# Kernel tuning notes

Hardware: AMD Instinct MI355X
Metric: run time of the kernel (lower is better)

## Reference

```python
import jax, jax.numpy as jnp
import numpy as np

# --- config (Qwen3-Next linear attention defaults) ---
B, S, H = 1, 256, 2048
NK, NV, DK, DV, K = 4, 32, 128, 128, 4
KEY_DIM = NK * DK          # 512
VAL_DIM = NV * DV          # 4096
CONV_DIM = 2 * KEY_DIM + VAL_DIM  # 5120
EPS = 1e-6


def setup_inputs() -> dict:
    key = jax.random.key(0)
    ks = jax.random.split(key, 8)
    rn = lambda k, shape, sc: jax.random.normal(k, shape, jnp.float32) * sc
    return {
        "hidden_states": jax.random.normal(ks[0], (B, S, H), jnp.float32),
        "w_qkvz": rn(ks[1], (2 * KEY_DIM + 2 * VAL_DIM, H), 0.02),  # in_proj_qkvz weight
        "w_ba": rn(ks[2], (2 * NV, H), 0.02),                        # in_proj_ba weight
        "w_out": rn(ks[3], (H, VAL_DIM), 0.02),                      # out_proj weight
        "conv_w": rn(ks[4], (CONV_DIM, 1, K), 0.1),                  # depthwise conv weight [C,1,K]
        "dt_bias": jnp.ones((NV,), jnp.float32),
        "A_log": jnp.zeros((NV,), jnp.float32),
        "norm_w": jnp.ones((DV,), jnp.float32),
    }


def reference(hidden_states, w_qkvz, w_ba, w_out, conv_w, dt_bias, A_log, norm_w):
    b, s, _ = hidden_states.shape
    # input projections (Linear without bias: x @ W.T)
    qkvz = hidden_states @ w_qkvz.T                      # [B,S,9216]
    ba = hidden_states @ w_ba.T                          # [B,S,64]
    q, k, v, z = jnp.split(qkvz, [KEY_DIM, 2 * KEY_DIM, 2 * KEY_DIM + VAL_DIM], axis=-1)
    beta, alpha = jnp.split(ba, 2, axis=-1)              # each [B,S,NV]

    # causal depthwise conv over concat(q,k,v), then silu
    qkv = jnp.concatenate([q, k, v], axis=-1).transpose(0, 2, 1)   # [B,C,S]
    qkv = jax.lax.conv_general_dilated(
        qkv, conv_w, window_strides=(1,), padding=[(K - 1, 0)],
        dimension_numbers=("NCH", "OIH", "NCH"), feature_group_count=CONV_DIM)
    qkv = jax.nn.silu(qkv).transpose(0, 2, 1)            # [B,S,C]
    q, k, v = jnp.split(qkv, [KEY_DIM, 2 * KEY_DIM], axis=-1)

    q = q.reshape(b, s, NK, DK)
    k = k.reshape(b, s, NK, DK)
    v = v.reshape(b, s, NV, DV)
    z = z.reshape(b, s, NV, DV)

    # GQA-style head expansion (repeat_interleave)
    ratio = NV // NK
    q = jnp.repeat(q, ratio, axis=2)                     # [B,S,NV,DK]
    k = jnp.repeat(k, ratio, axis=2)

    # NOTE: original computes g = -softplus(-A_log - alpha) but never uses it (dead code).
    beta_g = jax.nn.sigmoid(beta + dt_bias)[..., None]   # [B,S,NV,1]
    q = q * (DK ** -0.5)

    # naive delta-rule: full outer-product tensor + cumsum (memory-bound)
    kv = jnp.einsum("bsnk,bsnv->bsnkv", k, v * beta_g)   # [B,S,NV,DK,DV]
    out = jnp.einsum("bsnk,bsnkv->bsnv", q, jnp.cumsum(kv, axis=1))  # [B,S,NV,DV]

    # gated RMSNorm over head_v_dim in fp32
    of = out.astype(jnp.float32)
    var = jnp.mean(of * of, axis=-1, keepdims=True)
    of = of * jax.lax.rsqrt(var + EPS) * norm_w
    of = of * jax.nn.silu(z.astype(jnp.float32))

    return of.reshape(b, s, VAL_DIM) @ w_out.T           # [B,S,H]
```

## Files before the change

kernel.cpp:

```cpp
#include <hip/hip_runtime.h>
#include <hip/hip_bf16.h>

#define S_LEN   256
#define HID     2048
#define NVH     32
#define DKD     128
#define DVD     128
#define KEYDIM  512
#define VALDIM  4096
#define CONVDIM 5120
#define QKVZ_N  9216
#define EPS_F   1e-6f

typedef __attribute__((ext_vector_type(8))) short bf16x8;
typedef __attribute__((ext_vector_type(4))) float f32x4;

__device__ __forceinline__ unsigned short f2bf(float f) {
    union { float f; unsigned int i; } v; v.f = f;
    unsigned int x = v.i;
    return (unsigned short)((x + 0x7FFFu + ((x >> 16) & 1u)) >> 16);
}
__device__ __forceinline__ unsigned int pk2(float x, float y) {
    union { __hip_bfloat162 h; unsigned int u; } c;
    c.h = __float22bfloat162_rn(float2{x, y});
    return c.u;
}
__device__ __forceinline__ bf16x8 pack_bf8(float4 lo, float4 hi) {
    union { uint4 u; bf16x8 h; } c;
    c.u.x = pk2(lo.x, lo.y); c.u.y = pk2(lo.z, lo.w);
    c.u.z = pk2(hi.x, hi.y); c.u.w = pk2(hi.z, hi.w);
    return c.h;
}
__device__ __forceinline__ void gl_lds16(const void* g, void* l) {
    __builtin_amdgcn_global_load_lds(
        (const __attribute__((address_space(1))) unsigned int*)g,
        (__attribute__((address_space(3))) unsigned int*)l,
        16, 0, 0);
}

template<int NT>
__global__ __launch_bounds__(256, 2)
void gemm_db(const unsigned short* __restrict__ A, const float* __restrict__ B,
             float* __restrict__ Cpart, int N, int K, int kc) {
    __shared__ __align__(16) unsigned short As[2][128][64];
    __shared__ __align__(16) float Bs[2][NT][64];

    const int tid  = threadIdx.x;
    const int lane = tid & 63, wave = tid >> 6;
    const int wm = wave >> 1, wn = wave & 1;
    const int quad = lane >> 4, l16 = lane & 15;
    const int m0 = blockIdx.y * 128, n0 = blockIdx.x * NT;
    const int kbeg = blockIdx.z * kc;
    const int niter = kc >> 6;

    const int a_ro = lane >> 3;
    const int a_gc = (lane & 7) ^ a_ro;
    const int b_ro = lane >> 4;
    const int b_cs = lane & 15;

    f32x4 acc[4][2];
#pragma unroll
    for (int i = 0; i < 4; i++)
#pragma unroll
        for (int j = 0; j < 2; j++) acc[i][j] = (f32x4){0.f, 0.f, 0.f, 0.f};

    auto stage = [&](int buf, int kk) {
#pragma unroll
        for (int t = 0; t < 4; ++t) {
            int rbase = wave * 32 + t * 8;
            gl_lds16(A + (size_t)(m0 + rbase + a_ro) * K + kk + a_gc * 8,
                     &As[buf][rbase][0]);
        }
#pragma unroll
        for (int t = 0; t < NT / 16; ++t) {
            int rbase = wave * (NT / 4) + t * 4;
            int r = rbase + b_ro;
            int gc = b_cs ^ (r & 7);
            gl_lds16(B + (size_t)(n0 + r) * K + kk + gc * 4,
                     &Bs[buf][rbase][0]);
        }
    };

    auto compute = [&](int buf) {
#pragma unroll
        for (int ks = 0; ks < 2; ++ks) {
            bf16x8 af[4];
#pragma unroll
            for (int i = 0; i < 4; ++i) {
                int r = wm * 64 + i * 16 + l16;
                int c = (ks * 4 + quad) ^ (l16 & 7);
                af[i] = *(const bf16x8*)(&As[buf][r][c * 8]);
            }
#pragma unroll
            for (int j = 0; j < 2; ++j) {
                int r = wn * 32 + j * 16 + l16;
                int x = l16 & 7;
                int c0 = (ks * 8 + quad * 2) ^ x;
                int c1 = (ks * 8 + quad * 2 + 1) ^ x;
                float4 lo = *(const float4*)(&Bs[buf][r][c0 * 4]);
                float4 hi = *(const float4*)(&Bs[buf][r][c1 * 4]);
                bf16x8 bfr = pack_bf8(lo, hi);
#pragma unroll
                for (int i = 0; i < 4; ++i)
                    acc[i][j] = __builtin_amdgcn_mfma_f32_16x16x32_bf16(af[i], bfr, acc[i][j], 0, 0, 0);
            }
        }
    };

    stage(0, kbeg);
    __syncthreads();
    for (int it = 0; it < niter; ++it) {
        if (it + 1 < niter) stage((it + 1) & 1, kbeg + (it + 1) * 64);
        compute(it & 1);
        __syncthreads();
    }

    float* C = Cpart + (size_t)blockIdx.z * 256 * N;
#pragma unroll
    for (int i = 0; i < 4; i++)
#pragma unroll
        for (int j = 0; j < 2; j++)
#pragma unroll
            for (int r = 0; r < 4; r++) {
                int row = m0 + wm * 64 + i * 16 + quad * 4 + r;
                int col = n0 + wn * 32 + j * 16 + l16;
                C[(size_t)row * N + col] = acc[i][j][r];
            }
}

template<int P>
__global__ void reduce_sum(const float* __restrict__ part, float* __restrict__ out, int n) {
    int i = (blockIdx.x * 256 + threadIdx.x) * 4;
    if (i >= n) return;
    float4 s = *(const float4*)(part + i);
#pragma unroll
    for (int p = 1; p < P; p++) {
        float4 v = *(const float4*)(part + (size_t)p * n + i);
        s.x += v.x; s.y += v.y; s.z += v.z; s.w += v.w;
    }
    *(float4*)(out + i) = s;
}

__global__ __launch_bounds__(256)
void ba_proj_cvt(const float* __restrict__ hs, const float* __restrict__ w_ba,
                 float* __restrict__ ba, unsigned short* __restrict__ abf) {
    int s = blockIdx.x;
    int n = threadIdx.x & 63, seg = threadIdx.x >> 6;
    const float* x = hs + (size_t)s * HID + seg * 512;
    const float* w = w_ba + (size_t)n * HID + seg * 512;
    float acc = 0.f;
#pragma unroll 4
    for (int k = 0; k < 512; k += 4) {
        float4 xv = *(const float4*)(x + k);
        float4 wv = *(const float4*)(w + k);
        acc += xv.x * wv.x + xv.y * wv.y + xv.z * wv.z + xv.w * wv.w;
    }
    __shared__ float parts[4][64];
    parts[seg][n] = acc;
    {
        int d = threadIdx.x * 8;
        const float4* p = (const float4*)(hs + (size_t)s * HID + d);
        float4 a = p[0], b = p[1];
        uint4 r;
        r.x = pk2(a.x, a.y); r.y = pk2(a.z, a.w);
        r.z = pk2(b.x, b.y); r.w = pk2(b.z, b.w);
        *(uint4*)(abf + (size_t)s * HID + d) = r;
    }
    __syncthreads();
    if (threadIdx.x < 64)
        ba[s * 64 + threadIdx.x] = parts[0][threadIdx.x] + parts[1][threadIdx.x]
                                 + parts[2][threadIdx.x] + parts[3][threadIdx.x];
}

template<int P>
__global__ __launch_bounds__(256)
void sum_conv(const float* __restrict__ part, const float* __restrict__ conv_w,
              float* __restrict__ conv, float* __restrict__ zs) {
    const int s0 = blockIdx.y * 16;
    const int c  = blockIdx.x * 1024 + threadIdx.x * 4;
    auto sum4 = [&](int s) {
        const float* p = part + (size_t)s * QKVZ_N + c;
        float4 v = *(const float4*)p;
#pragma unroll
        for (int q = 1; q < P; q++) {
            float4 w = *(const float4*)(p + (size_t)q * S_LEN * QKVZ_N);
            v.x += w.x; v.y += w.y; v.z += w.z; v.w += w.w;
        }
        return v;
    };
    if (c < CONVDIM) {
        float4 cw[4];
#pragma unroll
        for (int i = 0; i < 4; ++i) cw[i] = *(const float4*)(conv_w + (size_t)(c + i) * 4);
        float4 w0{0,0,0,0}, w1{0,0,0,0}, w2{0,0,0,0};
        for (int s = (s0 >= 3 ? s0 - 3 : 0); s < s0; ++s) { w0 = w1; w1 = w2; w2 = sum4(s); }
        for (int s = s0; s < s0 + 16; ++s) {
            float4 w3 = sum4(s);
            float4 o;
            o.x = w0.x * cw[0].x + w1.x * cw[0].y + w2.x * cw[0].z + w3.x * cw[0].w;
            o.y = w0.y * cw[1].x + w1.y * cw[1].y + w2.y * cw[1].z + w3.y * cw[1].w;
            o.z = w0.z * cw[2].x + w1.z * cw[2].y + w2.z * cw[2].z + w3.z * cw[2].w;
            o.w = w0.w * cw[3].x + w1.w * cw[3].y + w2.w * cw[3].z + w3.w * cw[3].w;
            o.x = o.x / (1.f + __expf(-o.x));
            o.y = o.y / (1.f + __expf(-o.y));
            o.z = o.z / (1.f + __expf(-o.z));
            o.w = o.w / (1.f + __expf(-o.w));
            *(float4*)(conv + (size_t)s * CONVDIM + c) = o;
            w0 = w1; w1 = w2; w2 = w3;
        }
    } else {
        for (int s = s0; s < s0 + 16; ++s) {
            float4 v = sum4(s);
            *(float4*)(zs + (size_t)s * VALDIM + (c - CONVDIM)) = v;
        }
    }
}

__global__ __launch_bounds__(256)
void scores_k(const float* __restrict__ conv, const float* __restrict__ ba,
              const float* __restrict__ dt_bias, float* __restrict__ scores) {
    if (blockIdx.x > blockIdx.y) return;
    int hk = blockIdx.z;
    int s0 = blockIdx.y * 16, t0 = blockIdx.x * 16;
    __shared__ float Qs[16][132], Ks[16][132];
    int tid = threadIdx.x;
    int qoff = hk * DKD;
    int koff = KEYDIM + hk * DKD;
    for (int idx = tid; idx < 16 * 128; idx += 256) {
        int i = idx >> 7, d = idx & 127;
        Qs[i][d] = conv[(size_t)(s0 + i) * CONVDIM + qoff + d];
        Ks[i][d] = conv[(size_t)(t0 + i) * CONVDIM + koff + d];
    }
    __syncthreads();
    int tx = tid & 15, ty = tid >> 4;
    int s = s0 + ty, t = t0 + tx;
    float dot = 0.f;
    for (int d = 0; d < 128; d++) dot += Qs[ty][d] * Ks[tx][d];
    float base = (t <= s) ? dot * 0.08838834764831845f : 0.f;
#pragma unroll
    for (int v = 0; v < 8; v++) {
        int n = hk * 8 + v;
        float b = ba[t * 64 + n] + dt_bias[n];
        float bg = 1.f / (1.f + __expf(-b));
        scores[((size_t)n * 256 + s) * 256 + t] = base * bg;
    }
}

__global__ __launch_bounds__(256)
void attn_rms(const float* __restrict__ scores, const float* __restrict__ conv,
              const float* __restrict__ zs, const float* __restrict__ norm_w,
              unsigned short* __restrict__ normed) {
    int n = blockIdx.y, s0 = blockIdx.x * 16;
    int voff = 2 * KEYDIM + n * DVD;
    __shared__ float Ss[16][17];
    __shared__ float Vs[16][132];
    int tid = threadIdx.x, sy = tid >> 4, dx = tid & 15;
    float acc[8] = {0.f, 0.f, 0.f, 0.f, 0.f, 0.f, 0.f, 0.f};
    for (int t0 = 0; t0 <= s0; t0 += 16) {
        Ss[sy][dx] = scores[((size_t)n * 256 + s0 + sy) * 256 + t0 + dx];
        const float* vp = conv + (size_t)(t0 + sy) * CONVDIM + voff + dx * 8;
        *(float4*)&Vs[sy][dx * 8]     = *(const float4*)vp;
        *(float4*)&Vs[sy][dx * 8 + 4] = *(const float4*)(vp + 4);
        __syncthreads();
#pragma unroll
        for (int j = 0; j < 16; j++) {
            float sv = Ss[sy][j];
#pragma unroll
            for (int r = 0; r < 8; r++) acc[r] += sv * Vs[j][dx + 16 * r];
        }
        __syncthreads();
    }
    float ssq = 0.f;
#pragma unroll
    for (int r = 0; r < 8; r++) ssq += acc[r] * acc[r];
#pragma unroll
    for (int m = 1; m <= 8; m <<= 1) ssq += __shfl_xor(ssq, m, 64);
    float inv = rsqrtf(ssq * (1.f / 128.f) + EPS_F);
    int s = s0 + sy;
#pragma unroll
    for (int r = 0; r < 8; r++) {
        int d = dx + 16 * r;
        float z = zs[(size_t)s * VALDIM + n * DVD + d];
        float sz = z / (1.f + __expf(-z));
        float v = acc[r] * inv * norm_w[d] * sz;
        normed[((size_t)s * NVH + n) * DVD + d] = f2bf(v);
    }
}

extern "C" void kernel_launch(void* const* d_in, const int* in_sizes, int n_in,
                              void* d_out, int out_size, void* d_ws, size_t ws_size,
                              hipStream_t stream) {
    const float* hs      = (const float*)d_in[0];
    const float* w_qkvz  = (const float*)d_in[1];
    const float* w_ba    = (const float*)d_in[2];
    const float* w_out   = (const float*)d_in[3];
    const float* conv_w  = (const float*)d_in[4];
    const float* dt_bias = (const float*)d_in[5];
    const float* norm_w  = (const float*)d_in[7];

    char* ws = (char*)d_ws;
    unsigned short* abf = (unsigned short*)ws; ws += (size_t)S_LEN * HID * 2;
    float* ba   = (float*)ws;  ws += (size_t)S_LEN * 64 * 4;
    float* conv = (float*)ws;  ws += (size_t)S_LEN * CONVDIM * 4;
    float* zs   = (float*)ws;  ws += (size_t)S_LEN * VALDIM * 4;
    char* regB = ws;
    const bool big = ws_size >= (size_t)50 * 1024 * 1024;
    const int sk1 = big ? 4 : 2;
    const int sk2 = big ? 8 : 4;
    float* scratch1 = (float*)regB;
    unsigned short* normed = (unsigned short*)regB;
    float* scratch2 = (float*)(regB + 2097152);
    float* scores   = (float*)(regB + 2097152 + (size_t)sk2 * 2097152);

    ba_proj_cvt<<<S_LEN, 256, 0, stream>>>(hs, w_ba, ba, abf);
    gemm_db<64><<<dim3(QKVZ_N / 64, 2, sk1), 256, 0, stream>>>(abf, w_qkvz, scratch1, QKVZ_N, HID, HID / sk1);
    if (big) sum_conv<4><<<dim3(9, 16), 256, 0, stream>>>(scratch1, conv_w, conv, zs);
    else     sum_conv<2><<<dim3(9, 16), 256, 0, stream>>>(scratch1, conv_w, conv, zs);
    scores_k<<<dim3(16, 16, 4), 256, 0, stream>>>(conv, ba, dt_bias, scores);
    attn_rms<<<dim3(16, NVH), 256, 0, stream>>>(scores, conv, zs, norm_w, normed);
    gemm_db<64><<<dim3(HID / 64, 2, sk2), 256, 0, stream>>>(normed, w_out, scratch2, HID, VALDIM, VALDIM / sk2);
    if (big) reduce_sum<8><<<(S_LEN * HID) / 1024, 256, 0, stream>>>(scratch2, (float*)d_out, S_LEN * HID);
    else     reduce_sum<4><<<(S_LEN * HID) / 1024, 256, 0, stream>>>(scratch2, (float*)d_out, S_LEN * HID);
}
```

Before: 244.7 us.

## Stage GEMM B tile as bf16 via registers, remap grids, compact triangular scores launch

```diff
diff --git a/kernel.cpp b/kernel.cpp
--- a/kernel.cpp
+++ b/kernel.cpp
@@ -25,12 +25,6 @@
     c.h = __float22bfloat162_rn(float2{x, y});
     return c.u;
 }
-__device__ __forceinline__ bf16x8 pack_bf8(float4 lo, float4 hi) {
-    union { uint4 u; bf16x8 h; } c;
-    c.u.x = pk2(lo.x, lo.y); c.u.y = pk2(lo.z, lo.w);
-    c.u.z = pk2(hi.x, hi.y); c.u.w = pk2(hi.z, hi.w);
-    return c.h;
-}
 __device__ __forceinline__ void gl_lds16(const void* g, void* l) {
     __builtin_amdgcn_global_load_lds(
         (const __attribute__((address_space(1))) unsigned int*)g,
@@ -39,24 +33,27 @@
 }
 
 template<int NT>
-__global__ __launch_bounds__(256, 2)
+__global__ __launch_bounds__(256, 3)
 void gemm_db(const unsigned short* __restrict__ A, const float* __restrict__ B,
              float* __restrict__ Cpart, int N, int K, int kc) {
     __shared__ __align__(16) unsigned short As[2][128][64];
-    __shared__ __align__(16) float Bs[2][NT][64];
+    __shared__ __align__(16) unsigned short Bs[2][NT][64];
 
     const int tid  = threadIdx.x;
     const int lane = tid & 63, wave = tid >> 6;
     const int wm = wave >> 1, wn = wave & 1;
     const int quad = lane >> 4, l16 = lane & 15;
-    const int m0 = blockIdx.y * 128, n0 = blockIdx.x * NT;
-    const int kbeg = blockIdx.z * kc;
+    const int m0 = (blockIdx.x & 1) * 128;
+    const int n0 = (blockIdx.x >> 1) * NT;
+    const int kbeg = blockIdx.y * kc;
     const int niter = kc >> 6;
 
     const int a_ro = lane >> 3;
     const int a_gc = (lane & 7) ^ a_ro;
-    const int b_ro = lane >> 4;
-    const int b_cs = lane & 15;
+
+    const int rB = tid >> 2;
+    const int cB = (tid & 3) * 16;
+    const int swB = rB & 7;
 
     f32x4 acc[4][2];
 #pragma unroll
@@ -64,58 +61,67 @@
 #pragma unroll
         for (int j = 0; j < 2; j++) acc[i][j] = (f32x4){0.f, 0.f, 0.f, 0.f};
 
-    auto stage = [&](int buf, int kk) {
+    float4 br[4];
+    auto ldB = [&](int kk) {
+        const float* p = B + (size_t)(n0 + rB) * K + kk + cB;
+        br[0] = *(const float4*)(p);
+        br[1] = *(const float4*)(p + 4);
+        br[2] = *(const float4*)(p + 8);
+        br[3] = *(const float4*)(p + 12);
+    };
+    auto wrB = [&](int buf) {
+        uint4 u0, u1;
+        u0.x = pk2(br[0].x, br[0].y); u0.y = pk2(br[0].z, br[0].w);
+        u0.z = pk2(br[1].x, br[1].y); u0.w = pk2(br[1].z, br[1].w);
+        u1.x = pk2(br[2].x, br[2].y); u1.y = pk2(br[2].z, br[2].w);
+        u1.z = pk2(br[3].x, br[3].y); u1.w = pk2(br[3].z, br[3].w);
+        int c0 = ((tid & 3) * 2) ^ swB;
+        int c1 = ((tid & 3) * 2 + 1) ^ swB;
+        *(uint4*)(&Bs[buf][rB][c0 * 8]) = u0;
+        *(uint4*)(&Bs[buf][rB][c1 * 8]) = u1;
+    };
+    auto stageA = [&](int buf, int kk) {
 #pragma unroll
         for (int t = 0; t < 4; ++t) {
             int rbase = wave * 32 + t * 8;
             gl_lds16(A + (size_t)(m0 + rbase + a_ro) * K + kk + a_gc * 8,
                      &As[buf][rbase][0]);
         }
-#pragma unroll
-        for (int t = 0; t < NT / 16; ++t) {
-            int rbase = wave * (NT / 4) + t * 4;
-            int r = rbase + b_ro;
-            int gc = b_cs ^ (r & 7);
-            gl_lds16(B + (size_t)(n0 + r) * K + kk + gc * 4,
-                     &Bs[buf][rbase][0]);
-        }
-    };
-
+    };
     auto compute = [&](int buf) {
 #pragma unroll
         for (int ks = 0; ks < 2; ++ks) {
-            bf16x8 af[4];
-#pragma unroll
-            for (int i = 0; i < 4; ++i) {
-                int r = wm * 64 + i * 16 + l16;
-                int c = (ks * 4 + quad) ^ (l16 & 7);
-                af[i] = *(const bf16x8*)(&As[buf][r][c * 8]);
-            }
-#pragma unroll
-            for (int j = 0; j < 2; ++j) {
-                int r = wn * 32 + j * 16 + l16;
-                int x = l16 & 7;
-                int c0 = (ks * 8 + quad * 2) ^ x;
-                int c1 = (ks * 8 + quad * 2 + 1) ^ x;
-                float4 lo = *(const float4*)(&Bs[buf][r][c0 * 4]);
-                float4 hi = *(const float4*)(&Bs[buf][r][c1 * 4]);
-                bf16x8 bfr = pack_bf8(lo, hi);
-#pragma unroll
-                for (int i = 0; i < 4; ++i)
-                    acc[i][j] = __builtin_amdgcn_mfma_f32_16x16x32_bf16(af[i], bfr, acc[i][j], 0, 0, 0);
-            }
-        }
-    };
-
-    stage(0, kbeg);
+            bf16x8 af[4], bfr[2];
+            int c = ((ks * 4 + quad) ^ (l16 & 7)) * 8;
+#pragma unroll
+            for (int i = 0; i < 4; ++i)
+                af[i] = *(const bf16x8*)(&As[buf][wm * 64 + i * 16 + l16][c]);
+#pragma unroll
+            for (int j = 0; j < 2; ++j)
+                bfr[j] = *(const bf16x8*)(&Bs[buf][wn * 32 + j * 16 + l16][c]);
+#pragma unroll
+            for (int i = 0; i < 4; ++i)
+#pragma unroll
+                for (int j = 0; j < 2; ++j)
+                    acc[i][j] = __builtin_amdgcn_mfma_f32_16x16x32_bf16(af[i], bfr[j], acc[i][j], 0, 0, 0);
+        }
+    };
+
+    ldB(kbeg);
+    stageA(0, kbeg);
+    wrB(0);
+    if (niter > 1) ldB(kbeg + 64);
     __syncthreads();
+
     for (int it = 0; it < niter; ++it) {
-        if (it + 1 < niter) stage((it + 1) & 1, kbeg + (it + 1) * 64);
+        if (it + 1 < niter) stageA((it + 1) & 1, kbeg + (it + 1) * 64);
         compute(it & 1);
+        if (it + 1 < niter) wrB((it + 1) & 1);
+        if (it + 2 < niter) ldB(kbeg + (it + 2) * 64);
         __syncthreads();
     }
 
-    float* C = Cpart + (size_t)blockIdx.z * 256 * N;
+    float* C = Cpart + (size_t)blockIdx.y * 256 * N;
 #pragma unroll
     for (int i = 0; i < 4; i++)
 #pragma unroll
@@ -176,7 +182,7 @@
 __global__ __launch_bounds__(256)
 void sum_conv(const float* __restrict__ part, const float* __restrict__ conv_w,
               float* __restrict__ conv, float* __restrict__ zs) {
-    const int s0 = blockIdx.y * 16;
+    const int s0 = blockIdx.y * 8;
     const int c  = blockIdx.x * 1024 + threadIdx.x * 4;
     auto sum4 = [&](int s) {
         const float* p = part + (size_t)s * QKVZ_N + c;
@@ -194,7 +200,7 @@
         for (int i = 0; i < 4; ++i) cw[i] = *(const float4*)(conv_w + (size_t)(c + i) * 4);
         float4 w0{0,0,0,0}, w1{0,0,0,0}, w2{0,0,0,0};
         for (int s = (s0 >= 3 ? s0 - 3 : 0); s < s0; ++s) { w0 = w1; w1 = w2; w2 = sum4(s); }
-        for (int s = s0; s < s0 + 16; ++s) {
+        for (int s = s0; s < s0 + 8; ++s) {
             float4 w3 = sum4(s);
             float4 o;
             o.x = w0.x * cw[0].x + w1.x * cw[0].y + w2.x * cw[0].z + w3.x * cw[0].w;
@@ -209,7 +215,7 @@
             w0 = w1; w1 = w2; w2 = w3;
         }
     } else {
-        for (int s = s0; s < s0 + 16; ++s) {
+        for (int s = s0; s < s0 + 8; ++s) {
             float4 v = sum4(s);
             *(float4*)(zs + (size_t)s * VALDIM + (c - CONVDIM)) = v;
         }
@@ -219,9 +225,13 @@
 __global__ __launch_bounds__(256)
 void scores_k(const float* __restrict__ conv, const float* __restrict__ ba,
               const float* __restrict__ dt_bias, float* __restrict__ scores) {
-    if (blockIdx.x > blockIdx.y) return;
-    int hk = blockIdx.z;
-    int s0 = blockIdx.y * 16, t0 = blockIdx.x * 16;
+    int p = blockIdx.x;
+    int st = (int)((__fsqrt_rn(8.f * p + 1.f) - 1.f) * 0.5f);
+    while ((st + 1) * (st + 2) / 2 <= p) st++;
+    while (st * (st + 1) / 2 > p) st--;
+    int tt = p - st * (st + 1) / 2;
+    int hk = blockIdx.y;
+    int s0 = st * 16, t0 = tt * 16;
     __shared__ float Qs[16][132], Ks[16][132];
     int tid = threadIdx.x;
     int qoff = hk * DKD;
@@ -313,12 +323,12 @@
     float* scores   = (float*)(regB + 2097152 + (size_t)sk2 * 2097152);
 
     ba_proj_cvt<<<S_LEN, 256, 0, stream>>>(hs, w_ba, ba, abf);
-    gemm_db<64><<<dim3(QKVZ_N / 64, 2, sk1), 256, 0, stream>>>(abf, w_qkvz, scratch1, QKVZ_N, HID, HID / sk1);
-    if (big) sum_conv<4><<<dim3(9, 16), 256, 0, stream>>>(scratch1, conv_w, conv, zs);
-    else     sum_conv<2><<<dim3(9, 16), 256, 0, stream>>>(scratch1, conv_w, conv, zs);
-    scores_k<<<dim3(16, 16, 4), 256, 0, stream>>>(conv, ba, dt_bias, scores);
+    gemm_db<64><<<dim3(2 * (QKVZ_N / 64), sk1), 256, 0, stream>>>(abf, w_qkvz, scratch1, QKVZ_N, HID, HID / sk1);
+    if (big) sum_conv<4><<<dim3(9, 32), 256, 0, stream>>>(scratch1, conv_w, conv, zs);
+    else     sum_conv<2><<<dim3(9, 32), 256, 0, stream>>>(scratch1, conv_w, conv, zs);
+    scores_k<<<dim3(136, 4), 256, 0, stream>>>(conv, ba, dt_bias, scores);
     attn_rms<<<dim3(16, NVH), 256, 0, stream>>>(scores, conv, zs, norm_w, normed);
-    gemm_db<64><<<dim3(HID / 64, 2, sk2), 256, 0, stream>>>(normed, w_out, scratch2, HID, VALDIM, VALDIM / sk2);
+    gemm_db<64><<<dim3(2 * (HID / 64), sk2), 256, 0, stream>>>(normed, w_out, scratch2, HID, VALDIM, VALDIM / sk2);
     if (big) reduce_sum<8><<<(S_LEN * HID) / 1024, 256, 0, stream>>>(scratch2, (float*)d_out, S_LEN * HID);
     else     reduce_sum<4><<<(S_LEN * HID) / 1024, 256, 0, stream>>>(scratch2, (float*)d_out, S_LEN * HID);
 }
```

New measurement: 247.0 us. No clear change (+0.9%).
